# Kernel tuning notes

Hardware: AMD Instinct MI355X
Metric: run time of the kernel (lower is better)

Reference implementation:

```python
import jax, jax.numpy as jnp
import numpy as np

FILTERS = 128

def setup_inputs() -> dict:
    key = jax.random.key(0)
    ks = jax.random.split(key, 8)
    B, Nq, Nkv, C = 4, 4096, 4096, 128
    q_inputs = jax.random.normal(ks[0], (B, Nq, C), dtype=jnp.float32)
    kv_inputs = jax.random.normal(ks[1], (B, Nkv, C), dtype=jnp.float32)
    s = 1.0 / np.sqrt(C)
    Wq = jax.random.normal(ks[2], (C, FILTERS), dtype=jnp.float32) * s
    Wk = jax.random.normal(ks[3], (C, FILTERS), dtype=jnp.float32) * s
    Wv = jax.random.normal(ks[4], (C, FILTERS), dtype=jnp.float32) * s
    bq = jnp.zeros((FILTERS,), jnp.float32)
    bk = jnp.zeros((FILTERS,), jnp.float32)
    bv = jnp.zeros((FILTERS,), jnp.float32)
    return {"q_inputs": q_inputs, "kv_inputs": kv_inputs,
            "Wq": Wq, "bq": bq, "Wk": Wk, "bk": bk, "Wv": Wv, "bv": bv}

def reference(q_inputs, kv_inputs, Wq, bq, Wk, bk, Wv, bv):
    # Dense projections (last-axis matmul + bias)
    q = jnp.einsum('bnc,cf->bnf', q_inputs, Wq) + bq
    k = jnp.einsum('bmc,cf->bmf', kv_inputs, Wk) + bk
    v = jnp.einsum('bmc,cf->bmf', kv_inputs, Wv) + bv
    scale = jnp.sqrt(jnp.asarray(FILTERS, jnp.float32))
    scores = jnp.einsum('bnf,bmf->bnm', q, k) / scale  # [B, Nq, Nkv]
    weights = jax.nn.softmax(scores, axis=-1)
    return jnp.einsum('bnm,bmf->bnf', weights, v)
```

## Files before the change

### kernel.cpp

```cpp
#include <hip/hip_runtime.h>
#include <stdint.h>
#include <math.h>

typedef unsigned short u16;
typedef unsigned int u32;
typedef __bf16 bf16x8 __attribute__((ext_vector_type(8)));
typedef unsigned short u16x8 __attribute__((ext_vector_type(8)));
typedef unsigned short u16x4 __attribute__((ext_vector_type(4)));
typedef float f32x4 __attribute__((ext_vector_type(4)));
typedef float f32x16 __attribute__((ext_vector_type(16)));

#define MFMA16(a, b, c) __builtin_amdgcn_mfma_f32_16x16x32_bf16((a), (b), (c), 0, 0, 0)
#define MFMA32(a, b, c) __builtin_amdgcn_mfma_f32_32x32x16_bf16((a), (b), (c), 0, 0, 0)

__device__ __forceinline__ u16 f2b(float f) {
    union { unsigned int i; float f; } v; v.f = f;
    unsigned int r = (v.i + 0x7FFFu + ((v.i >> 16) & 1u)) >> 16;
    return (u16)r;
}
__device__ __forceinline__ u32 cvtpk(float lo, float hi) {
    u32 r; asm("v_cvt_pk_bf16_f32 %0, %1, %2" : "=v"(r) : "v"(lo), "v"(hi));
    return r;
}
__device__ __forceinline__ void gload16(const void* g, void* l) {
    __builtin_amdgcn_global_load_lds(
        (const __attribute__((address_space(1))) u32*)g,
        (__attribute__((address_space(3))) u32*)l, 16, 0, 0);
}

constexpr int N = 4096;
constexpr int Cc = 128;
constexpr int Fc = 128;
constexpr int BATCH = 4;
constexpr int NT = N / 128;

constexpr int XS_STRIDE = 136;
constexpr int WT_STRIDE = 136;
constexpr int KO_STRIDE = 136;
constexpr int VO_STRIDE = 72;
constexpr int OM_STRIDE = 130;

#define QSCALE 0.12751744750f

__global__ __launch_bounds__(256) void wtrans_kernel(
    const float* __restrict__ Wq, const float* __restrict__ Wk,
    const float* __restrict__ Wv, u16* __restrict__ WtG)
{
    __shared__ __align__(16) u16 Wl[128 * 132];
    const int tid = threadIdx.x;
    const int which = blockIdx.x;
    const float* W = which == 0 ? Wq : (which == 1 ? Wk : Wv);
#pragma unroll
    for (int it = 0; it < 16; ++it) {
        int idx4 = tid + it * 256; int e0 = idx4 * 4;
        int c = e0 >> 7, f = e0 & 127;
        float4 wv = *(const float4*)(W + e0);
        u16x4 h; h[0] = f2b(wv.x); h[1] = f2b(wv.y); h[2] = f2b(wv.z); h[3] = f2b(wv.w);
        *(u16x4*)&Wl[c * 132 + f] = h;
    }
    __syncthreads();
    u16* out = WtG + which * 16384;
#pragma unroll
    for (int it = 0; it < 8; ++it) {
        int idx8 = tid + it * 256; int e0 = idx8 * 8;
        int f = e0 >> 7, c = e0 & 127;
        u16x8 h;
#pragma unroll
        for (int j = 0; j < 8; ++j) h[j] = Wl[(c + j) * 132 + f];
        *(u16x8*)(out + e0) = h;
    }
}

__global__ __launch_bounds__(256) void proj_kernel(
    const float* __restrict__ q_in, const float* __restrict__ kv_in,
    const u16* __restrict__ WtG,
    const float* __restrict__ bq, const float* __restrict__ bk,
    const float* __restrict__ bv,
    u16* __restrict__ Qw, u16* __restrict__ Kw, u16* __restrict__ Vtw)
{
    __shared__ __align__(16) u16 Xs[64 * XS_STRIDE];
    __shared__ __align__(16) u16 Wt[128 * WT_STRIDE];

    const int tid = threadIdx.x;
    const int which = blockIdx.y;
    const int b = blockIdx.z;
    const int m0 = blockIdx.x * 64;

    const float* X = (which == 0 ? q_in : kv_in) + ((size_t)b * N + m0) * Cc;
    const u16* Wsrc = WtG + which * 16384;
    const float* bias = which == 0 ? bq : (which == 1 ? bk : bv);

#pragma unroll
    for (int it = 0; it < 8; ++it) {
        int idx4 = tid + it * 256; int e0 = idx4 * 4;
        int r = e0 >> 7, c = e0 & 127;
        float4 xv = *(const float4*)(X + e0);
        u16x4 h; h[0] = f2b(xv.x); h[1] = f2b(xv.y); h[2] = f2b(xv.z); h[3] = f2b(xv.w);
        *(u16x4*)&Xs[r * XS_STRIDE + c] = h;
    }
#pragma unroll
    for (int it = 0; it < 8; ++it) {
        int idx8 = tid + it * 256; int e0 = idx8 * 8;
        int f = e0 >> 7, c = e0 & 127;
        *(u16x8*)&Wt[f * WT_STRIDE + c] = *(const u16x8*)(Wsrc + e0);
    }
    __syncthreads();

    const int lane = tid & 63;
    const int w = tid >> 6;
    const int n16 = lane & 15;
    const int quad = lane >> 4;

    if (which < 2) {
        bf16x8 ax[4];
#pragma unroll
        for (int kk = 0; kk < 4; ++kk)
            ax[kk] = *(const bf16x8*)&Xs[(w * 16 + n16) * XS_STRIDE + kk * 32 + quad * 8];
        const float scale = (which == 0) ? QSCALE : 1.0f;
        if (which == 0) {
#pragma unroll
            for (int ft = 0; ft < 8; ++ft) {
                f32x4 acc = {0.f, 0.f, 0.f, 0.f};
#pragma unroll
                for (int kk = 0; kk < 4; ++kk) {
                    bf16x8 bw = *(const bf16x8*)&Wt[(ft * 16 + n16) * WT_STRIDE + kk * 32 + quad * 8];
                    acc = MFMA16(ax[kk], bw, acc);
                }
                float bias_f = bias[ft * 16 + n16];
#pragma unroll
                for (int r = 0; r < 4; ++r) {
                    int row = m0 + w * 16 + quad * 4 + r;
                    Qw[((size_t)b * N + row) * Fc + ft * 16 + n16] =
                        f2b((acc[r] + bias_f) * scale);
                }
            }
        } else {
            float accs[8][4];
            float biasf[8];
#pragma unroll
            for (int ft = 0; ft < 8; ++ft) {
                f32x4 acc = {0.f, 0.f, 0.f, 0.f};
#pragma unroll
                for (int kk = 0; kk < 4; ++kk) {
                    bf16x8 bw = *(const bf16x8*)&Wt[(ft * 16 + n16) * WT_STRIDE + kk * 32 + quad * 8];
                    acc = MFMA16(ax[kk], bw, acc);
                }
                biasf[ft] = bias[ft * 16 + n16];
#pragma unroll
                for (int r = 0; r < 4; ++r) accs[ft][r] = acc[r];
            }
            __syncthreads();
            u16* const Ko = Xs;
#pragma unroll
            for (int ft = 0; ft < 8; ++ft)
#pragma unroll
                for (int r = 0; r < 4; ++r) {
                    int rl = w * 16 + quad * 4 + r;
                    int f = ft * 16 + n16;
                    Ko[rl * KO_STRIDE + f] = f2b(accs[ft][r] + biasf[ft]);
                }
            __syncthreads();
            u16* const outK = Kw + ((size_t)b * 1024 + (m0 >> 5) * 8) * 512;
#pragma unroll
            for (int it = 0; it < 4; ++it) {
                int e = tid * 8 + it * 2048;
                int lg = e >> 12, rem = e & 4095;
                int kk2 = rem >> 9, rem2 = rem & 511;
                int hig = rem2 >> 8, l31v = (rem2 >> 3) & 31;
                int row_l = lg * 32 + l31v;
                int fbase = kk2 * 16 + hig * 8;
                *(u16x8*)(outK + e) = *(const u16x8*)&Ko[row_l * KO_STRIDE + fbase];
            }
        }
    } else {
        float accs[2][4][4];
        float bias4[2][4];
#pragma unroll
        for (int ft2 = 0; ft2 < 2; ++ft2) {
            int ftg = w * 2 + ft2;
            bf16x8 aw[4];
#pragma unroll
            for (int kk = 0; kk < 4; ++kk)
                aw[kk] = *(const bf16x8*)&Wt[(ftg * 16 + n16) * WT_STRIDE + kk * 32 + quad * 8];
#pragma unroll
            for (int r = 0; r < 4; ++r) bias4[ft2][r] = bias[ftg * 16 + quad * 4 + r];
#pragma unroll
            for (int nt = 0; nt < 4; ++nt) {
                f32x4 acc = {0.f, 0.f, 0.f, 0.f};
#pragma unroll
                for (int kk = 0; kk < 4; ++kk) {
                    bf16x8 bx = *(const bf16x8*)&Xs[(nt * 16 + n16) * XS_STRIDE + kk * 32 + quad * 8];
                    acc = MFMA16(aw[kk], bx, acc);
                }
#pragma unroll
                for (int r = 0; r < 4; ++r) accs[ft2][nt][r] = acc[r];
            }
        }
        __syncthreads();
        u16* const Vo = Wt;
#pragma unroll
        for (int ft2 = 0; ft2 < 2; ++ft2)
#pragma unroll
            for (int nt = 0; nt < 4; ++nt)
#pragma unroll
                for (int r = 0; r < 4; ++r) {
                    int fg = (w * 2 + ft2) * 16 + quad * 4 + r;
                    int kl = nt * 16 + n16;
                    Vo[fg * VO_STRIDE + kl] = f2b(accs[ft2][nt][r] + bias4[ft2][r]);
                }
        __syncthreads();
        u16* const outV = Vtw + ((size_t)b * 1024 + (m0 >> 5) * 8) * 512;
#pragma unroll
        for (int it = 0; it < 4; ++it) {
            int e = tid * 8 + it * 2048;
            int lg = e >> 12, rem = e & 4095;
            int grp = rem >> 9, rem2 = rem & 511;
            int cb = grp >> 1, ks = grp & 1;
            int hig = rem2 >> 8, l31v = (rem2 >> 3) & 31;
            int ch = cb * 32 + l31v;
            int kbase = lg * 32 + ks * 16 + hig * 8;
            *(u16x8*)(outV + e) = *(const u16x8*)&Vo[ch * VO_STRIDE + kbase];
        }
    }
}

__global__ __launch_bounds__(512, 2) void attn_kernel(
    const u16* __restrict__ Qw, const u16* __restrict__ Kw,
    const u16* __restrict__ Vtw, float* __restrict__ out)
{
    __shared__ __align__(16) char smem[134144];
    u16* const B0 = (u16*)smem;
    u16* const B1 = (u16*)(smem + 65536);

    const int tid = threadIdx.x;
    const int id = blockIdx.x + 64 * blockIdx.y;
    const int b = (id >> 1) & 3;
    const int q0 = (((id & 1) << 5) + (id >> 3)) << 6;

    const int lane = tid & 63;
    const int w = tid >> 6;
    const int kg = w & 3;
    const int qg = w >> 2;
    const int l31 = lane & 31;
    const int hi = lane >> 5;

    bf16x8 aq[8];
    {
        const u16* qp = Qw + ((size_t)b * N + q0 + qg * 32 + l31) * Cc + hi * 8;
#pragma unroll
        for (int kk = 0; kk < 8; ++kk) aq[kk] = *(const bf16x8*)(qp + kk * 16);
    }

    const u16* const Ktile = Kw + (size_t)b * 1024 * 512;
    const u16* const Vtile = Vtw + (size_t)b * 1024 * 512;
    const int kro = kg * 4096 + lane * 8;
    const int vro = kg * 4096 + lane * 8;

    f32x16 o[4];
#pragma unroll
    for (int cb = 0; cb < 4; ++cb)
#pragma unroll
        for (int i = 0; i < 16; ++i) o[cb][i] = 0.f;
    float lloc = 0.f;

    int ci[4];
#pragma unroll
    for (int it = 0; it < 4; ++it) ci[it] = tid + it * 512;

    auto STAGE = [&](u16* bd, int t) {
        const u16* ksrc = Ktile + (size_t)t * 16384;
        const u16* vsrc = Vtile + (size_t)t * 16384;
#pragma unroll
        for (int it = 0; it < 4; ++it)
            gload16(ksrc + ci[it] * 8, bd + ci[it] * 8);
#pragma unroll
        for (int it = 0; it < 4; ++it)
            gload16(vsrc + ci[it] * 8, bd + 16384 + ci[it] * 8);
    };

    auto COMPUTE = [&](const u16* buf) {
        const u16* Ksb = buf;
        const u16* Vsb = buf + 16384;
        f32x16 st;
#pragma unroll
        for (int i = 0; i < 16; ++i) st[i] = 0.f;
        __builtin_amdgcn_s_setprio(1);
#pragma unroll
        for (int kk = 0; kk < 8; ++kk) {
            bf16x8 ak = *(const bf16x8*)(Ksb + kro + kk * 512);
            st = MFMA32(ak, aq[kk], st);
        }
        __builtin_amdgcn_s_setprio(0);
        float p[16];
#pragma unroll
        for (int i = 0; i < 16; ++i) p[i] = exp2f(st[i]);
        lloc += ((((p[0] + p[1]) + (p[2] + p[3])) + ((p[4] + p[5]) + (p[6] + p[7])))
               + (((p[8] + p[9]) + (p[10] + p[11])) + ((p[12] + p[13]) + (p[14] + p[15]))));
        bf16x8 pb[2];
#pragma unroll
        for (int ks = 0; ks < 2; ++ks) {
            u32 a0 = cvtpk(p[ks * 8 + 0], p[ks * 8 + 1]);
            u32 a1 = cvtpk(p[ks * 8 + 2], p[ks * 8 + 3]);
            u32 a2 = cvtpk(p[ks * 8 + 4], p[ks * 8 + 5]);
            u32 a3 = cvtpk(p[ks * 8 + 6], p[ks * 8 + 7]);
            auto s02 = __builtin_amdgcn_permlane32_swap(a0, a2, false, false);
            auto s13 = __builtin_amdgcn_permlane32_swap(a1, a3, false, false);
            union { u32 u[4]; bf16x8 v; } bb;
            bb.u[0] = s02[0]; bb.u[1] = s13[0]; bb.u[2] = s02[1]; bb.u[3] = s13[1];
            pb[ks] = bb.v;
        }
        __builtin_amdgcn_s_setprio(1);
#pragma unroll
        for (int cb = 0; cb < 4; ++cb) {
            bf16x8 av0 = *(const bf16x8*)(Vsb + vro + (cb * 2 + 0) * 512);
            bf16x8 av1 = *(const bf16x8*)(Vsb + vro + (cb * 2 + 1) * 512);
            o[cb] = MFMA32(av0, pb[0], o[cb]);
            o[cb] = MFMA32(av1, pb[1], o[cb]);
        }
        __builtin_amdgcn_s_setprio(0);
    };

    STAGE(B0, 0);
    __syncthreads();
    for (int t = 0; t < NT; t += 2) {
        if (t + 1 < NT) STAGE(B1, t + 1);
        COMPUTE(B0);
        __syncthreads();
        if (t + 2 < NT) STAGE(B0, t + 2);
        COMPUTE(B1);
        __syncthreads();
    }

    float lv = lloc + __shfl_xor(lloc, 32);

    float* const Om = (float*)smem;
    float* const Lm = (float*)(smem + 4 * 64 * OM_STRIDE * 4);

    const int qrow_w = qg * 32 + l31;
    const int crow0 = 4 * hi;
    {
        float* dst = Om + (size_t)(kg * 64 + qrow_w) * OM_STRIDE;
#pragma unroll
        for (int cb = 0; cb < 4; ++cb)
#pragma unroll
            for (int i = 0; i < 16; ++i) {
                int ch = cb * 32 + (i & 3) + 8 * (i >> 2) + crow0;
                dst[ch] = o[cb][i];
            }
        if (hi == 0) Lm[kg * 64 + qrow_w] = lv;
    }
    __syncthreads();

    const int qrow = tid >> 3;
    const int ch0 = (tid & 7) * 16;
    const float lsum = Lm[qrow] + Lm[64 + qrow] + Lm[128 + qrow] + Lm[192 + qrow];
    const float linv = 1.0f / lsum;
    float* op = out + ((size_t)b * N + q0 + qrow) * Fc + ch0;
#pragma unroll
    for (int j4 = 0; j4 < 4; ++j4) {
        f32x4 v;
#pragma unroll
        for (int jj = 0; jj < 4; ++jj) {
            int ch = ch0 + j4 * 4 + jj;
            float s = Om[(size_t)(0 * 64 + qrow) * OM_STRIDE + ch]
                    + Om[(size_t)(1 * 64 + qrow) * OM_STRIDE + ch]
                    + Om[(size_t)(2 * 64 + qrow) * OM_STRIDE + ch]
                    + Om[(size_t)(3 * 64 + qrow) * OM_STRIDE + ch];
            v[jj] = s * linv;
        }
        *(f32x4*)(op + j4 * 4) = v;
    }
}

extern "C" void kernel_launch(void* const* d_in, const int* in_sizes, int n_in,
                              void* d_out, int out_size, void* d_ws, size_t ws_size,
                              hipStream_t stream) {
    (void)in_sizes; (void)n_in; (void)out_size; (void)ws_size;
    const float* q_in  = (const float*)d_in[0];
    const float* kv_in = (const float*)d_in[1];
    const float* Wq = (const float*)d_in[2];
    const float* bq = (const float*)d_in[3];
    const float* Wk = (const float*)d_in[4];
    const float* bk = (const float*)d_in[5];
    const float* Wv = (const float*)d_in[6];
    const float* bv = (const float*)d_in[7];

    const size_t qkv = (size_t)BATCH * N * Fc;
    u16* Qw  = (u16*)d_ws;
    u16* Kw  = Qw + qkv;
    u16* Vtw = Kw + qkv;
    u16* WtG = Vtw + qkv;

    wtrans_kernel<<<dim3(3), dim3(256), 0, stream>>>(Wq, Wk, Wv, WtG);
    proj_kernel<<<dim3(64, 3, BATCH), dim3(256), 0, stream>>>(
        q_in, kv_in, WtG, bq, bk, bv, Qw, Kw, Vtw);
    attn_kernel<<<dim3(64, BATCH), dim3(512), 0, stream>>>(
        Qw, Kw, Vtw, (float*)d_out);
}
```

Baseline: 134.6 us.

## Fuse weight transpose, projections and attention into one persistent kernel with grid barrier

Merges the three launches (weight transpose, QKV projection, attention) into one kernel. Each block transposes all three weights itself, projects its own 64-row slice of Q, K and V, and keeps its Q tile in shared memory so Q never round-trips through global memory. K and V are still written to the workspace and made visible through a software grid barrier (atomic counter with sleep-polling) before attention starts. This removes two launch gaps and the Q write and read, but every block now repeats the weight transpose, the barrier needs all 256 blocks to be co-resident, and shared memory per block grows to about 148 KB.

```diff
diff --git a/kernel.cpp b/kernel.cpp
--- a/kernel.cpp
+++ b/kernel.cpp
@@ -33,223 +33,240 @@
 constexpr int Fc = 128;
 constexpr int BATCH = 4;
 constexpr int NT = N / 128;
-
-constexpr int XS_STRIDE = 136;
-constexpr int WT_STRIDE = 136;
-constexpr int KO_STRIDE = 136;
-constexpr int VO_STRIDE = 72;
+constexpr int NBLK = 256;
+
+constexpr int WL_S  = 132;
+constexpr int WT_S  = 136;
+constexpr int X_S   = 136;
+constexpr int KO_S  = 136;
+constexpr int VO_S  = 72;
+constexpr int QLS_S = 132;
 constexpr int OM_STRIDE = 130;
 
 #define QSCALE 0.12751744750f
 
-__global__ __launch_bounds__(256) void wtrans_kernel(
-    const float* __restrict__ Wq, const float* __restrict__ Wk,
-    const float* __restrict__ Wv, u16* __restrict__ WtG)
+__global__ __launch_bounds__(512, 2) void fused_kernel(
+    const float* __restrict__ q_in, const float* __restrict__ kv_in,
+    const float* __restrict__ Wq, const float* __restrict__ bq,
+    const float* __restrict__ Wk, const float* __restrict__ bk,
+    const float* __restrict__ Wv, const float* __restrict__ bv,
+    u16* __restrict__ Kw, u16* __restrict__ Vtw,
+    int* __restrict__ bar, float* __restrict__ out)
 {
-    __shared__ __align__(16) u16 Wl[128 * 132];
+    __shared__ __align__(16) char smem[147968];
+    u16* const Wl  = (u16*)(smem);
+    u16* const Wt  = (u16*)(smem + 33792);
+    u16* const Xq  = (u16*)(smem + 68608);
+    u16* const Xkv = (u16*)(smem + 86016);
+    u16* const Ko  = (u16*)(smem + 68608);
+    u16* const Vo  = (u16*)(smem);
+    u16* const Qls = (u16*)(smem + 131072);
+
     const int tid = threadIdx.x;
-    const int which = blockIdx.x;
-    const float* W = which == 0 ? Wq : (which == 1 ? Wk : Wv);
-#pragma unroll
-    for (int it = 0; it < 16; ++it) {
-        int idx4 = tid + it * 256; int e0 = idx4 * 4;
-        int c = e0 >> 7, f = e0 & 127;
-        float4 wv = *(const float4*)(W + e0);
-        u16x4 h; h[0] = f2b(wv.x); h[1] = f2b(wv.y); h[2] = f2b(wv.z); h[3] = f2b(wv.w);
-        *(u16x4*)&Wl[c * 132 + f] = h;
-    }
-    __syncthreads();
-    u16* out = WtG + which * 16384;
-#pragma unroll
-    for (int it = 0; it < 8; ++it) {
-        int idx8 = tid + it * 256; int e0 = idx8 * 8;
-        int f = e0 >> 7, c = e0 & 127;
-        u16x8 h;
-#pragma unroll
-        for (int j = 0; j < 8; ++j) h[j] = Wl[(c + j) * 132 + f];
-        *(u16x8*)(out + e0) = h;
-    }
-}
-
-__global__ __launch_bounds__(256) void proj_kernel(
-    const float* __restrict__ q_in, const float* __restrict__ kv_in,
-    const u16* __restrict__ WtG,
-    const float* __restrict__ bq, const float* __restrict__ bk,
-    const float* __restrict__ bv,
-    u16* __restrict__ Qw, u16* __restrict__ Kw, u16* __restrict__ Vtw)
-{
-    __shared__ __align__(16) u16 Xs[64 * XS_STRIDE];
-    __shared__ __align__(16) u16 Wt[128 * WT_STRIDE];
-
-    const int tid = threadIdx.x;
-    const int which = blockIdx.y;
-    const int b = blockIdx.z;
-    const int m0 = blockIdx.x * 64;
-
-    const float* X = (which == 0 ? q_in : kv_in) + ((size_t)b * N + m0) * Cc;
-    const u16* Wsrc = WtG + which * 16384;
-    const float* bias = which == 0 ? bq : (which == 1 ? bk : bv);
-
-#pragma unroll
-    for (int it = 0; it < 8; ++it) {
-        int idx4 = tid + it * 256; int e0 = idx4 * 4;
-        int r = e0 >> 7, c = e0 & 127;
-        float4 xv = *(const float4*)(X + e0);
-        u16x4 h; h[0] = f2b(xv.x); h[1] = f2b(xv.y); h[2] = f2b(xv.z); h[3] = f2b(xv.w);
-        *(u16x4*)&Xs[r * XS_STRIDE + c] = h;
-    }
-#pragma unroll
-    for (int it = 0; it < 8; ++it) {
-        int idx8 = tid + it * 256; int e0 = idx8 * 8;
-        int f = e0 >> 7, c = e0 & 127;
-        *(u16x8*)&Wt[f * WT_STRIDE + c] = *(const u16x8*)(Wsrc + e0);
-    }
-    __syncthreads();
+    const int id = blockIdx.x + 64 * blockIdx.y;
+    const int b = (id >> 1) & 3;
+    const int m0 = (((id & 1) << 5) + (id >> 3)) << 6;
 
     const int lane = tid & 63;
     const int w = tid >> 6;
     const int n16 = lane & 15;
     const int quad = lane >> 4;
 
-    if (which < 2) {
+    {
+        const float* Xg = q_in  + ((size_t)b * N + m0) * Cc;
+        const float* Xk = kv_in + ((size_t)b * N + m0) * Cc;
+#pragma unroll
+        for (int it = 0; it < 4; ++it) {
+            int idx4 = tid + it * 512; int e0 = idx4 * 4;
+            int r = e0 >> 7, c = e0 & 127;
+            float4 xv = *(const float4*)(Xg + e0);
+            u16x4 h; h[0] = f2b(xv.x); h[1] = f2b(xv.y); h[2] = f2b(xv.z); h[3] = f2b(xv.w);
+            *(u16x4*)&Xq[r * X_S + c] = h;
+            float4 kv = *(const float4*)(Xk + e0);
+            u16x4 g; g[0] = f2b(kv.x); g[1] = f2b(kv.y); g[2] = f2b(kv.z); g[3] = f2b(kv.w);
+            *(u16x4*)&Xkv[r * X_S + c] = g;
+        }
+    }
+
+    auto STAGE_W = [&](const float* W) {
+#pragma unroll
+        for (int it = 0; it < 8; ++it) {
+            int idx4 = tid + it * 512; int e0 = idx4 * 4;
+            int c = e0 >> 7, f = e0 & 127;
+            float4 wv = *(const float4*)(W + e0);
+            u16x4 h; h[0] = f2b(wv.x); h[1] = f2b(wv.y); h[2] = f2b(wv.z); h[3] = f2b(wv.w);
+            *(u16x4*)&Wl[c * WL_S + f] = h;
+        }
+    };
+    auto TRANS_W = [&]() {
+#pragma unroll
+        for (int it = 0; it < 4; ++it) {
+            int idx8 = tid + it * 512; int e0 = idx8 * 8;
+            int f = e0 >> 7, c = e0 & 127;
+            u16x8 h;
+#pragma unroll
+            for (int j = 0; j < 8; ++j) h[j] = Wl[(c + j) * WL_S + f];
+            *(u16x8*)&Wt[f * WT_S + c] = h;
+        }
+    };
+
+    const int msub = w & 3;
+    const int ftb  = (w >> 2) * 4;
+
+    STAGE_W(Wq);
+    __syncthreads();
+    TRANS_W();
+    __syncthreads();
+    {
         bf16x8 ax[4];
 #pragma unroll
         for (int kk = 0; kk < 4; ++kk)
-            ax[kk] = *(const bf16x8*)&Xs[(w * 16 + n16) * XS_STRIDE + kk * 32 + quad * 8];
-        const float scale = (which == 0) ? QSCALE : 1.0f;
-        if (which == 0) {
-#pragma unroll
-            for (int ft = 0; ft < 8; ++ft) {
-                f32x4 acc = {0.f, 0.f, 0.f, 0.f};
-#pragma unroll
-                for (int kk = 0; kk < 4; ++kk) {
-                    bf16x8 bw = *(const bf16x8*)&Wt[(ft * 16 + n16) * WT_STRIDE + kk * 32 + quad * 8];
-                    acc = MFMA16(ax[kk], bw, acc);
-                }
-                float bias_f = bias[ft * 16 + n16];
-#pragma unroll
-                for (int r = 0; r < 4; ++r) {
-                    int row = m0 + w * 16 + quad * 4 + r;
-                    Qw[((size_t)b * N + row) * Fc + ft * 16 + n16] =
-                        f2b((acc[r] + bias_f) * scale);
-                }
-            }
-        } else {
-            float accs[8][4];
-            float biasf[8];
-#pragma unroll
-            for (int ft = 0; ft < 8; ++ft) {
-                f32x4 acc = {0.f, 0.f, 0.f, 0.f};
-#pragma unroll
-                for (int kk = 0; kk < 4; ++kk) {
-                    bf16x8 bw = *(const bf16x8*)&Wt[(ft * 16 + n16) * WT_STRIDE + kk * 32 + quad * 8];
-                    acc = MFMA16(ax[kk], bw, acc);
-                }
-                biasf[ft] = bias[ft * 16 + n16];
-#pragma unroll
-                for (int r = 0; r < 4; ++r) accs[ft][r] = acc[r];
-            }
-            __syncthreads();
-            u16* const Ko = Xs;
-#pragma unroll
-            for (int ft = 0; ft < 8; ++ft)
-#pragma unroll
-                for (int r = 0; r < 4; ++r) {
-                    int rl = w * 16 + quad * 4 + r;
-                    int f = ft * 16 + n16;
-                    Ko[rl * KO_STRIDE + f] = f2b(accs[ft][r] + biasf[ft]);
-                }
-            __syncthreads();
-            u16* const outK = Kw + ((size_t)b * 1024 + (m0 >> 5) * 8) * 512;
-#pragma unroll
-            for (int it = 0; it < 4; ++it) {
-                int e = tid * 8 + it * 2048;
-                int lg = e >> 12, rem = e & 4095;
-                int kk2 = rem >> 9, rem2 = rem & 511;
-                int hig = rem2 >> 8, l31v = (rem2 >> 3) & 31;
-                int row_l = lg * 32 + l31v;
-                int fbase = kk2 * 16 + hig * 8;
-                *(u16x8*)(outK + e) = *(const u16x8*)&Ko[row_l * KO_STRIDE + fbase];
-            }
-        }
-    } else {
-        float accs[2][4][4];
-        float bias4[2][4];
-#pragma unroll
-        for (int ft2 = 0; ft2 < 2; ++ft2) {
-            int ftg = w * 2 + ft2;
-            bf16x8 aw[4];
-#pragma unroll
-            for (int kk = 0; kk < 4; ++kk)
-                aw[kk] = *(const bf16x8*)&Wt[(ftg * 16 + n16) * WT_STRIDE + kk * 32 + quad * 8];
-#pragma unroll
-            for (int r = 0; r < 4; ++r) bias4[ft2][r] = bias[ftg * 16 + quad * 4 + r];
-#pragma unroll
-            for (int nt = 0; nt < 4; ++nt) {
-                f32x4 acc = {0.f, 0.f, 0.f, 0.f};
-#pragma unroll
-                for (int kk = 0; kk < 4; ++kk) {
-                    bf16x8 bx = *(const bf16x8*)&Xs[(nt * 16 + n16) * XS_STRIDE + kk * 32 + quad * 8];
-                    acc = MFMA16(aw[kk], bx, acc);
-                }
-#pragma unroll
-                for (int r = 0; r < 4; ++r) accs[ft2][nt][r] = acc[r];
-            }
-        }
-        __syncthreads();
-        u16* const Vo = Wt;
-#pragma unroll
-        for (int ft2 = 0; ft2 < 2; ++ft2)
-#pragma unroll
-            for (int nt = 0; nt < 4; ++nt)
-#pragma unroll
-                for (int r = 0; r < 4; ++r) {
-                    int fg = (w * 2 + ft2) * 16 + quad * 4 + r;
-                    int kl = nt * 16 + n16;
-                    Vo[fg * VO_STRIDE + kl] = f2b(accs[ft2][nt][r] + bias4[ft2][r]);
-                }
-        __syncthreads();
+            ax[kk] = *(const bf16x8*)&Xq[(msub * 16 + n16) * X_S + kk * 32 + quad * 8];
+#pragma unroll
+        for (int f2 = 0; f2 < 4; ++f2) {
+            int ft = ftb + f2;
+            f32x4 acc = {0.f, 0.f, 0.f, 0.f};
+#pragma unroll
+            for (int kk = 0; kk < 4; ++kk) {
+                bf16x8 bw = *(const bf16x8*)&Wt[(ft * 16 + n16) * WT_S + kk * 32 + quad * 8];
+                acc = MFMA16(ax[kk], bw, acc);
+            }
+            float bias_f = bq[ft * 16 + n16];
+#pragma unroll
+            for (int r = 0; r < 4; ++r) {
+                int rl = msub * 16 + quad * 4 + r;
+                Qls[rl * QLS_S + ft * 16 + n16] = f2b((acc[r] + bias_f) * QSCALE);
+            }
+        }
+    }
+    __syncthreads();
+
+    STAGE_W(Wk);
+    __syncthreads();
+    TRANS_W();
+    __syncthreads();
+    {
+        bf16x8 ax[4];
+#pragma unroll
+        for (int kk = 0; kk < 4; ++kk)
+            ax[kk] = *(const bf16x8*)&Xkv[(msub * 16 + n16) * X_S + kk * 32 + quad * 8];
+        float accs[4][4]; float biasf[4];
+#pragma unroll
+        for (int f2 = 0; f2 < 4; ++f2) {
+            int ft = ftb + f2;
+            f32x4 acc = {0.f, 0.f, 0.f, 0.f};
+#pragma unroll
+            for (int kk = 0; kk < 4; ++kk) {
+                bf16x8 bw = *(const bf16x8*)&Wt[(ft * 16 + n16) * WT_S + kk * 32 + quad * 8];
+                acc = MFMA16(ax[kk], bw, acc);
+            }
+            biasf[f2] = bk[ft * 16 + n16];
+#pragma unroll
+            for (int r = 0; r < 4; ++r) accs[f2][r] = acc[r];
+        }
+#pragma unroll
+        for (int f2 = 0; f2 < 4; ++f2)
+#pragma unroll
+            for (int r = 0; r < 4; ++r) {
+                int rl = msub * 16 + quad * 4 + r;
+                int f = (ftb + f2) * 16 + n16;
+                Ko[rl * KO_S + f] = f2b(accs[f2][r] + biasf[f2]);
+            }
+    }
+    __syncthreads();
+    {
+        u16* const outK = Kw + ((size_t)b * 1024 + (m0 >> 5) * 8) * 512;
+#pragma unroll
+        for (int it = 0; it < 2; ++it) {
+            int e = tid * 8 + it * 4096;
+            int lg = e >> 12, rem = e & 4095;
+            int kk2 = rem >> 9, rem2 = rem & 511;
+            int hig = rem2 >> 8, l31v = (rem2 >> 3) & 31;
+            int rl = lg * 32 + l31v;
+            int fb = kk2 * 16 + hig * 8;
+            *(u16x8*)(outK + e) = *(const u16x8*)&Ko[rl * KO_S + fb];
+        }
+    }
+    __syncthreads();
+
+    STAGE_W(Wv);
+    __syncthreads();
+    TRANS_W();
+    __syncthreads();
+    {
+        const int ftg = w;
+        bf16x8 aw[4];
+#pragma unroll
+        for (int kk = 0; kk < 4; ++kk)
+            aw[kk] = *(const bf16x8*)&Wt[(ftg * 16 + n16) * WT_S + kk * 32 + quad * 8];
+        float bias4[4];
+#pragma unroll
+        for (int r = 0; r < 4; ++r) bias4[r] = bv[ftg * 16 + quad * 4 + r];
+        float accs[4][4];
+#pragma unroll
+        for (int nt = 0; nt < 4; ++nt) {
+            f32x4 acc = {0.f, 0.f, 0.f, 0.f};
+#pragma unroll
+            for (int kk = 0; kk < 4; ++kk) {
+                bf16x8 bx = *(const bf16x8*)&Xkv[(nt * 16 + n16) * X_S + kk * 32 + quad * 8];
+                acc = MFMA16(aw[kk], bx, acc);
+            }
+#pragma unroll
+            for (int r = 0; r < 4; ++r) accs[nt][r] = acc[r];
+        }
+#pragma unroll
+        for (int nt = 0; nt < 4; ++nt)
+#pragma unroll
+            for (int r = 0; r < 4; ++r) {
+                int fg = ftg * 16 + quad * 4 + r;
+                int kl = nt * 16 + n16;
+                Vo[fg * VO_S + kl] = f2b(accs[nt][r] + bias4[r]);
+            }
+    }
+    __syncthreads();
+    {
         u16* const outV = Vtw + ((size_t)b * 1024 + (m0 >> 5) * 8) * 512;
 #pragma unroll
-        for (int it = 0; it < 4; ++it) {
-            int e = tid * 8 + it * 2048;
+        for (int it = 0; it < 2; ++it) {
+            int e = tid * 8 + it * 4096;
             int lg = e >> 12, rem = e & 4095;
             int grp = rem >> 9, rem2 = rem & 511;
             int cb = grp >> 1, ks = grp & 1;
             int hig = rem2 >> 8, l31v = (rem2 >> 3) & 31;
             int ch = cb * 32 + l31v;
-            int kbase = lg * 32 + ks * 16 + hig * 8;
-            *(u16x8*)(outV + e) = *(const u16x8*)&Vo[ch * VO_STRIDE + kbase];
-        }
-    }
-}
-
-__global__ __launch_bounds__(512, 2) void attn_kernel(
-    const u16* __restrict__ Qw, const u16* __restrict__ Kw,
-    const u16* __restrict__ Vtw, float* __restrict__ out)
-{
-    __shared__ __align__(16) char smem[134144];
+            int kb = lg * 32 + ks * 16 + hig * 8;
+            *(u16x8*)(outV + e) = *(const u16x8*)&Vo[ch * VO_S + kb];
+        }
+    }
+
+    __syncthreads();
+    __threadfence();
+    if (tid == 0) {
+        atomicAdd(bar, 1);
+        int v = atomicAdd(bar, 0);
+        int guard = 0;
+        while (v < NBLK && guard < (1 << 18)) {
+            __builtin_amdgcn_s_sleep(8);
+            v = atomicAdd(bar, 0);
+            ++guard;
+        }
+    }
+    __syncthreads();
+    __threadfence();
+
     u16* const B0 = (u16*)smem;
     u16* const B1 = (u16*)(smem + 65536);
 
-    const int tid = threadIdx.x;
-    const int id = blockIdx.x + 64 * blockIdx.y;
-    const int b = (id >> 1) & 3;
-    const int q0 = (((id & 1) << 5) + (id >> 3)) << 6;
-
-    const int lane = tid & 63;
-    const int w = tid >> 6;
     const int kg = w & 3;
     const int qg = w >> 2;
     const int l31 = lane & 31;
     const int hi = lane >> 5;
+    const int q0 = m0;
 
     bf16x8 aq[8];
-    {
-        const u16* qp = Qw + ((size_t)b * N + q0 + qg * 32 + l31) * Cc + hi * 8;
-#pragma unroll
-        for (int kk = 0; kk < 8; ++kk) aq[kk] = *(const bf16x8*)(qp + kk * 16);
-    }
+#pragma unroll
+    for (int kk = 0; kk < 8; ++kk)
+        aq[kk] = *(const bf16x8*)&Qls[(qg * 32 + l31) * QLS_S + hi * 8 + kk * 16];
 
     const u16* const Ktile = Kw + (size_t)b * 1024 * 512;
     const u16* const Vtile = Vtw + (size_t)b * 1024 * 512;
@@ -386,14 +403,11 @@
     const float* bv = (const float*)d_in[7];
 
     const size_t qkv = (size_t)BATCH * N * Fc;
-    u16* Qw  = (u16*)d_ws;
-    u16* Kw  = Qw + qkv;
+    u16* Kw  = (u16*)d_ws;
     u16* Vtw = Kw + qkv;
-    u16* WtG = Vtw + qkv;
-
-    wtrans_kernel<<<dim3(3), dim3(256), 0, stream>>>(Wq, Wk, Wv, WtG);
-    proj_kernel<<<dim3(64, 3, BATCH), dim3(256), 0, stream>>>(
-        q_in, kv_in, WtG, bq, bk, bv, Qw, Kw, Vtw);
-    attn_kernel<<<dim3(64, BATCH), dim3(512), 0, stream>>>(
-        Qw, Kw, Vtw, (float*)d_out);
+    int* bar = (int*)((char*)d_ws + 2 * qkv * sizeof(u16));
+
+    hipMemsetAsync(bar, 0, 128, stream);
+    fused_kernel<<<dim3(64, BATCH), dim3(512), 0, stream>>>(
+        q_in, kv_in, Wq, bq, Wk, bk, Wv, bv, Kw, Vtw, bar, (float*)d_out);
 }
```

Result: slower. 206.3 us (+53.2%).
